# Performance work log

Measured on AMD Instinct MI355X. Metric: run time of the kernel, lower is better.

## Reference

```python
import jax, jax.numpy as jnp
import numpy as np
from jax.ops import segment_sum

N_NODES = 100000
N_EDGES = 3200000
NUM_FEATURES = 256


def setup_inputs() -> dict:
    key = jax.random.key(0)
    ks = jax.random.split(key, 12)
    def lin(k, fan_in, fan_out):
        bound = 1.0 / np.sqrt(fan_in)
        kw, kb = jax.random.split(k)
        W = jax.random.uniform(kw, (fan_in, fan_out), jnp.float32, -bound, bound)
        b = jax.random.uniform(kb, (fan_out,), jnp.float32, -bound, bound)
        return W, b
    x = jax.random.normal(ks[0], (N_NODES, NUM_FEATURES), jnp.float32)
    edge_index = jax.random.randint(ks[1], (2, N_EDGES), 0, N_NODES, jnp.int64 if jax.config.jax_enable_x64 else jnp.int32)
    W1, b1 = lin(ks[2], NUM_FEATURES, 64)
    W2, b2 = lin(ks[3], 64, 32)
    W3, b3 = lin(ks[4], 32, 16)
    Ws02, bs02 = lin(ks[5], NUM_FEATURES, 32)
    Ws03, bs03 = lin(ks[6], NUM_FEATURES, 16)
    Ws13, bs13 = lin(ks[7], 64, 16)
    Wout, bout = lin(ks[8], 16, 1)
    return dict(x=x, edge_index=edge_index, W1=W1, b1=b1, W2=W2, b2=b2,
                W3=W3, b3=b3, Ws02=Ws02, bs02=bs02, Ws03=Ws03, bs03=bs03,
                Ws13=Ws13, bs13=bs13, Wout=Wout, bout=bout)


def _deg_inv_sqrt(edge_index, n_nodes):
    # gcn_norm with self-loops: degree counted at target nodes, +1 for self-loop
    dst = edge_index[1]
    deg = segment_sum(jnp.ones(edge_index.shape[1], jnp.float32), dst, num_segments=n_nodes) + 1.0
    return jnp.where(deg > 0, jax.lax.rsqrt(deg), 0.0)


def _gcn_conv(x, W, b, edge_index, dinv):
    # PyG GCNConv: h = x W; out[i] = sum_{j->i} dinv[j]*dinv[i]*h[j] + dinv[i]^2*h[i] + b
    src, dst = edge_index[0], edge_index[1]
    h = x @ W                                   # [N, out]
    norm = (dinv[src] * dinv[dst])[:, None]     # [E, 1]
    agg = segment_sum(h[src] * norm, dst, num_segments=x.shape[0])
    agg = agg + (dinv * dinv)[:, None] * h      # self-loop term
    return agg + b


def reference(x, edge_index, W1, b1, W2, b2, W3, b3,
              Ws02, bs02, Ws03, bs03, Ws13, bs13, Wout, bout):
    # Dropout in eval mode (identity).
    dinv = _deg_inv_sqrt(edge_index, x.shape[0])
    x1 = jax.nn.relu(_gcn_conv(x, W1, b1, edge_index, dinv))
    x2 = jax.nn.relu(_gcn_conv(x1, W2, b2, edge_index, dinv) + x @ Ws02 + bs02)
    x3 = jax.nn.relu(_gcn_conv(x2, W3, b3, edge_index, dinv)
                     + x @ Ws03 + bs03 + x1 @ Ws13 + bs13)
    return jax.nn.sigmoid(x3 @ Wout + bout)
```

## Files before the change

kernel.cpp:

```cpp
#include <hip/hip_runtime.h>
#include <hip/hip_bf16.h>
#include <math.h>


#define NBUCK_MAX 512
#define P1_CHUNK 8192
#define EPT 32
#define BCAP 9216

typedef __attribute__((ext_vector_type(8))) short bfrag;
typedef __attribute__((ext_vector_type(4))) float f4_t;

__device__ inline float uaf(unsigned u) { return __uint_as_float(u); }
__device__ inline ushort f2bf(float f) {
    __hip_bfloat16 b = __float2bfloat16(f);
    return *reinterpret_cast<ushort*>(&b);
}


__global__ __launch_bounds__(256) void bucket_hist_kernel(
    const int* __restrict__ dst, int E, int* __restrict__ bucket_count, int nbuckets)
{
    __shared__ int lhist[NBUCK_MAX];
    for (int i = threadIdx.x; i < nbuckets; i += 256) lhist[i] = 0;
    __syncthreads();
    const int stride = gridDim.x * 256;
    for (int e = blockIdx.x * 256 + threadIdx.x; e < E; e += stride)
        atomicAdd(&lhist[dst[e] >> 8], 1);
    __syncthreads();
    for (int i = threadIdx.x; i < nbuckets; i += 256) {
        int c = lhist[i];
        if (c) atomicAdd(&bucket_count[i], c);
    }
}

__global__ __launch_bounds__(512) void bucket_scan_kernel(
    const int* __restrict__ bucket_count, int* __restrict__ bucket_base,
    int* __restrict__ bucket_cursor, int nbuckets)
{
    __shared__ int tmp[512];
    const int tid = threadIdx.x;
    int v = (tid < nbuckets) ? bucket_count[tid] : 0;
    tmp[tid] = v;
    __syncthreads();
    for (int off = 1; off < 512; off <<= 1) {
        int t = (tid >= off) ? tmp[tid - off] : 0;
        __syncthreads();
        tmp[tid] += t;
        __syncthreads();
    }
    if (tid < nbuckets) {
        int base = tmp[tid] - v;
        bucket_base[tid]   = base;
        bucket_cursor[tid] = base;
    }
}

__global__ __launch_bounds__(256) void partition_kernel(
    const int* __restrict__ src, const int* __restrict__ dst, int E,
    int* __restrict__ bucket_cursor, unsigned int* __restrict__ keys, int nbuckets)
{
    __shared__ int hist[NBUCK_MAX];
    __shared__ int lofs[NBUCK_MAX];
    __shared__ int gbase[NBUCK_MAX];
    __shared__ int lcur[NBUCK_MAX];
    __shared__ int ssum[256];
    __shared__ unsigned int stage[P1_CHUNK];
    __shared__ int gidx[P1_CHUNK];

    const int tid = threadIdx.x;
    const int e0  = blockIdx.x * P1_CHUNK;
    const int nE  = min(P1_CHUNK, E - e0);

    for (int i = tid; i < NBUCK_MAX; i += 256) { hist[i] = 0; lcur[i] = 0; }
    __syncthreads();

    int myb[EPT];
    unsigned int mypk[EPT];
#pragma unroll
    for (int j = 0; j < EPT; ++j) {
        const int e = e0 + tid + j * 256;
        if (e < E) {
            const int d = dst[e];
            myb[j]  = d >> 8;
            mypk[j] = ((unsigned int)(d & 255) << 17) | (unsigned int)src[e];
            atomicAdd(&hist[myb[j]], 1);
        } else myb[j] = -1;
    }
    __syncthreads();

    int a0 = (2 * tid     < nbuckets) ? hist[2 * tid]     : 0;
    int a1 = (2 * tid + 1 < nbuckets) ? hist[2 * tid + 1] : 0;
    ssum[tid] = a0 + a1;
    __syncthreads();
    for (int off = 1; off < 256; off <<= 1) {
        int t = (tid >= off) ? ssum[tid - off] : 0;
        __syncthreads();
        ssum[tid] += t;
        __syncthreads();
    }
    const int ex = ssum[tid] - (a0 + a1);
    if (2 * tid     < nbuckets) lofs[2 * tid]     = ex;
    if (2 * tid + 1 < nbuckets) lofs[2 * tid + 1] = ex + a0;
    __syncthreads();

    for (int i = tid; i < nbuckets; i += 256)
        gbase[i] = atomicAdd(&bucket_cursor[i], hist[i]);
    __syncthreads();

#pragma unroll
    for (int j = 0; j < EPT; ++j) {
        if (myb[j] >= 0) {
            const int b = myb[j];
            const int l = lofs[b] + atomicAdd(&lcur[b], 1);
            stage[l] = mypk[j];
            gidx[l]  = gbase[b] - lofs[b] + l;
        }
    }
    __syncthreads();

    for (int i = tid; i < nE; i += 256)
        keys[gidx[i]] = stage[i];
}

__global__ __launch_bounds__(256) void csr_build_kernel(
    const unsigned int* __restrict__ keys, const int* __restrict__ bucket_base,
    const int* __restrict__ bucket_count,
    int* __restrict__ row_off, float* __restrict__ dinv, int* __restrict__ col,
    int N, int E)
{
    __shared__ unsigned int inb[BCAP];
    __shared__ int outv[BCAP];
    __shared__ int hist[256];
    __shared__ int lofs[256];
    __shared__ int ssum[256];

    const int tid  = threadIdx.x;
    const int b    = blockIdx.x;
    const int base = bucket_base[b];
    const int cnt  = min(bucket_count[b], BCAP);
    const int n0   = b << 8;
    const int nn   = min(256, N - n0);

    for (int i = tid; i < cnt; i += 256) inb[i] = keys[base + i];
    hist[tid] = 0;
    __syncthreads();

    for (int i = tid; i < cnt; i += 256)
        atomicAdd(&hist[inb[i] >> 17], 1);
    __syncthreads();

    ssum[tid] = hist[tid];
    __syncthreads();
    for (int off = 1; off < 256; off <<= 1) {
        int t = (tid >= off) ? ssum[tid - off] : 0;
        __syncthreads();
        ssum[tid] += t;
        __syncthreads();
    }
    lofs[tid] = ssum[tid] - hist[tid];

    if (tid < nn) {
        row_off[n0 + tid] = base + lofs[tid];
        dinv[n0 + tid]    = rsqrtf((float)hist[tid] + 1.0f);
    }
    if (b == 0 && tid == 0) row_off[N] = E;
    __syncthreads();

    hist[tid] = 0;
    __syncthreads();

    for (int i = tid; i < cnt; i += 256) {
        const unsigned int k = inb[i];
        const int node = k >> 17;
        const int l = lofs[node] + atomicAdd(&hist[node], 1);
        outv[l] = (int)(k & 0x1FFFF);
    }
    __syncthreads();

    for (int i = tid; i < cnt; i += 256)
        col[base + i] = outv[i];
}


__global__ __launch_bounds__(256) void prep_weights_kernel(
    const float* __restrict__ W1, const float* __restrict__ Ws02,
    const float* __restrict__ Ws03, const float* __restrict__ W2,
    const float* __restrict__ Ws13, const float* __restrict__ W3,
    ushort* __restrict__ Wt0, ushort* __restrict__ Wt1, ushort* __restrict__ Wt2)
{
    int idx = blockIdx.x * 256 + threadIdx.x;
    if (idx < 32768) {
        int f = idx >> 8, k = idx & 255;
        float v = 0.f;
        if (f < 64)       v = W1[k * 64 + f];
        else if (f < 96)  v = Ws02[k * 32 + (f - 64)];
        else if (f < 112) v = Ws03[k * 16 + (f - 96)];
        Wt0[idx] = f2bf(v);
    } else if (idx < 32768 + 3072) {
        int t = idx - 32768;
        int f = t >> 6, k = t & 63;
        float v = (f < 32) ? W2[k * 32 + f] : Ws13[k * 16 + (f - 32)];
        Wt1[t] = f2bf(v);
    } else if (idx < 32768 + 3072 + 512) {
        int t = idx - 32768 - 3072;
        int f = t >> 5, k = t & 31;
        Wt2[t] = f2bf(W3[k * 16 + f]);
    }
}


__global__ __launch_bounds__(256, 4) void gemm_mfma0(
    const float* __restrict__ X, const ushort* __restrict__ Wt0,
    const float* __restrict__ bs02, const float* __restrict__ bs03,
    const float* __restrict__ dinv,
    __hip_bfloat16* __restrict__ g1, float* __restrict__ pre2,
    float* __restrict__ pre3, int N)
{
    constexpr int LDA = 40;
    __shared__ ushort As[2][128 * LDA];

    const int tid  = threadIdx.x;
    const int lane = tid & 63;
    const int wave = tid >> 6;
    const int n0   = blockIdx.x * 128;

    const int srow = tid >> 1;
    const int sq   = (tid & 1) * 4;
    const float* xrow = (n0 + srow < N) ? &X[(size_t)(n0 + srow) * 256] : nullptr;

    float4 pf[4];
#pragma unroll
    for (int j = 0; j < 4; ++j)
        pf[j] = xrow ? *reinterpret_cast<const float4*>(&xrow[(sq + j) * 4])
                     : make_float4(0.f, 0.f, 0.f, 0.f);

    f4_t acc[4][4];
#pragma unroll
    for (int a = 0; a < 4; ++a)
#pragma unroll
        for (int b = 0; b < 4; ++b) acc[a][b] = {0.f, 0.f, 0.f, 0.f};

    const int wm = wave & 1, wf = wave >> 1;
    const int mrow = (lane & 15);
    const int kq   = (lane >> 4) * 8;

    {
        ushort* dst = &As[0][srow * LDA + sq * 4];
#pragma unroll
        for (int j = 0; j < 4; ++j) {
            ushort4 cv;
            cv.x = f2bf(pf[j].x); cv.y = f2bf(pf[j].y);
            cv.z = f2bf(pf[j].z); cv.w = f2bf(pf[j].w);
            *reinterpret_cast<ushort4*>(&dst[j * 4]) = cv;
        }
    }
    __syncthreads();

    for (int panel = 0; panel < 8; ++panel) {
        const int kc = panel * 32;
        const int buf = panel & 1;

        if (panel < 7) {
#pragma unroll
            for (int j = 0; j < 4; ++j)
                pf[j] = xrow ? *reinterpret_cast<const float4*>(
                                   &xrow[(panel + 1) * 32 + (sq + j) * 4])
                             : make_float4(0.f, 0.f, 0.f, 0.f);
        }

        bfrag bfr[4];
#pragma unroll
        for (int ft = 0; ft < 4; ++ft) {
            const uint4 raw = *reinterpret_cast<const uint4*>(
                &Wt0[(size_t)(wf * 64 + ft * 16 + mrow) * 256 + kc + kq]);
            bfr[ft] = *reinterpret_cast<const bfrag*>(&raw);
        }
        bfrag af[4];
#pragma unroll
        for (int mt = 0; mt < 4; ++mt)
            af[mt] = *reinterpret_cast<const bfrag*>(
                &As[buf][(wm * 64 + mt * 16 + mrow) * LDA + kq]);
#pragma unroll
        for (int mt = 0; mt < 4; ++mt)
#pragma unroll
            for (int ft = 0; ft < 4; ++ft)
                acc[mt][ft] = __builtin_amdgcn_mfma_f32_16x16x32_bf16(
                    af[mt], bfr[ft], acc[mt][ft], 0, 0, 0);

        if (panel < 7) {
            ushort* dst = &As[1 - buf][srow * LDA + sq * 4];
#pragma unroll
            for (int j = 0; j < 4; ++j) {
                ushort4 cv;
                cv.x = f2bf(pf[j].x); cv.y = f2bf(pf[j].y);
                cv.z = f2bf(pf[j].z); cv.w = f2bf(pf[j].w);
                *reinterpret_cast<ushort4*>(&dst[j * 4]) = cv;
            }
            __syncthreads();
        }
    }

#pragma unroll
    for (int mt = 0; mt < 4; ++mt) {
#pragma unroll
        for (int ft = 0; ft < 4; ++ft) {
            const int fg = wf * 64 + ft * 16 + mrow;
#pragma unroll
            for (int r = 0; r < 4; ++r) {
                const int n = n0 + wm * 64 + mt * 16 + (lane >> 4) * 4 + r;
                if (n >= N) continue;
                const float a = acc[mt][ft][r];
                if (fg < 64) {
                    g1[(size_t)n * 64 + fg] = __float2bfloat16(dinv[n] * a);
                } else if (fg < 96) {
                    pre2[(size_t)n * 32 + (fg - 64)] = a + bs02[fg - 64];
                } else if (fg < 112) {
                    pre3[(size_t)n * 16 + (fg - 96)] = a + bs03[fg - 96];
                }
            }
        }
    }
}

__global__ __launch_bounds__(256) void gemm_mfma1(
    const ushort* __restrict__ X1, const ushort* __restrict__ Wt1,
    const float* __restrict__ bs13, const float* __restrict__ dinv,
    __hip_bfloat16* __restrict__ g2, float* __restrict__ pre3, int N)
{
    constexpr int LDA = 72;
    __shared__ ushort As[128 * LDA];

    const int tid  = threadIdx.x;
    const int lane = tid & 63;
    const int wave = tid >> 6;
    const int n0   = blockIdx.x * 128;

    for (int idx = tid; idx < 1024; idx += 256) {
        const int row = idx >> 3, c = idx & 7;
        const int n = n0 + row;
        uint4 v = make_uint4(0, 0, 0, 0);
        if (n < N) v = *reinterpret_cast<const uint4*>(&X1[(size_t)n * 64 + c * 8]);
        *reinterpret_cast<uint4*>(&As[row * LDA + c * 8]) = v;
    }
    __syncthreads();

    f4_t acc[2][3];
#pragma unroll
    for (int a = 0; a < 2; ++a)
#pragma unroll
        for (int b = 0; b < 3; ++b) acc[a][b] = {0.f, 0.f, 0.f, 0.f};

    const int m0 = wave * 32;
    const int mrow = lane & 15;
    const int kq   = (lane >> 4) * 8;
#pragma unroll
    for (int p = 0; p < 2; ++p) {
        bfrag af[2], bfr[3];
#pragma unroll
        for (int mt = 0; mt < 2; ++mt)
            af[mt] = *reinterpret_cast<const bfrag*>(
                &As[(m0 + mt * 16 + mrow) * LDA + p * 32 + kq]);
#pragma unroll
        for (int ft = 0; ft < 3; ++ft) {
            const uint4 raw = *reinterpret_cast<const uint4*>(
                &Wt1[(size_t)(ft * 16 + mrow) * 64 + p * 32 + kq]);
            bfr[ft] = *reinterpret_cast<const bfrag*>(&raw);
        }
#pragma unroll
        for (int mt = 0; mt < 2; ++mt)
#pragma unroll
            for (int ft = 0; ft < 3; ++ft)
                acc[mt][ft] = __builtin_amdgcn_mfma_f32_16x16x32_bf16(
                    af[mt], bfr[ft], acc[mt][ft], 0, 0, 0);
    }

#pragma unroll
    for (int mt = 0; mt < 2; ++mt) {
#pragma unroll
        for (int ft = 0; ft < 3; ++ft) {
            const int fg = ft * 16 + mrow;
#pragma unroll
            for (int r = 0; r < 4; ++r) {
                const int n = n0 + m0 + mt * 16 + (lane >> 4) * 4 + r;
                if (n >= N) continue;
                const float a = acc[mt][ft][r];
                if (fg < 32) {
                    g2[(size_t)n * 32 + fg] = __float2bfloat16(dinv[n] * a);
                } else {
                    pre3[(size_t)n * 16 + (fg - 32)] += a + bs13[fg - 32];
                }
            }
        }
    }
}

__global__ __launch_bounds__(256) void gemm_mfma2(
    const ushort* __restrict__ X2, const ushort* __restrict__ Wt2,
    const float* __restrict__ dinv, __hip_bfloat16* __restrict__ g3, int N)
{
    constexpr int LDA = 40;
    __shared__ ushort As[256 * LDA];

    const int tid  = threadIdx.x;
    const int lane = tid & 63;
    const int wave = tid >> 6;
    const int n0   = blockIdx.x * 256;

    for (int idx = tid; idx < 1024; idx += 256) {
        const int row = idx >> 2, c = idx & 3;
        const int n = n0 + row;
        uint4 v = make_uint4(0, 0, 0, 0);
        if (n < N) v = *reinterpret_cast<const uint4*>(&X2[(size_t)n * 32 + c * 8]);
        *reinterpret_cast<uint4*>(&As[row * LDA + c * 8]) = v;
    }
    __syncthreads();

    f4_t acc[4];
#pragma unroll
    for (int a = 0; a < 4; ++a) acc[a] = {0.f, 0.f, 0.f, 0.f};

    const int m0 = wave * 64;
    const int mrow = lane & 15;
    const int kq   = (lane >> 4) * 8;
    const uint4 raw = *reinterpret_cast<const uint4*>(&Wt2[(size_t)mrow * 32 + kq]);
    const bfrag bfr = *reinterpret_cast<const bfrag*>(&raw);
#pragma unroll
    for (int mt = 0; mt < 4; ++mt) {
        const bfrag af = *reinterpret_cast<const bfrag*>(
            &As[(m0 + mt * 16 + mrow) * LDA + kq]);
        acc[mt] = __builtin_amdgcn_mfma_f32_16x16x32_bf16(af, bfr, acc[mt], 0, 0, 0);
    }

#pragma unroll
    for (int mt = 0; mt < 4; ++mt) {
#pragma unroll
        for (int r = 0; r < 4; ++r) {
            const int n = n0 + m0 + mt * 16 + (lane >> 4) * 4 + r;
            if (n >= N) continue;
            g3[(size_t)n * 16 + mrow] = __float2bfloat16(dinv[n] * acc[mt][r]);
        }
    }
}


template<int F, int MODE>
__global__ __launch_bounds__(256) void agg_kernel(
    const ushort* __restrict__ g, const float* __restrict__ dinv,
    const int* __restrict__ row_off, const int* __restrict__ col,
    const float* __restrict__ bias, const float* __restrict__ pre,
    const float* __restrict__ Wout, const float* __restrict__ bout,
    void* __restrict__ out, int N)
{
    constexpr int FG  = F / 4;
    constexpr int EPW = 64 / FG;
    constexpr int U   = (F == 64) ? 4 : (F == 32 ? 2 : 1);

    const int lane = threadIdx.x & 63;
    const int wv   = threadIdx.x >> 6;
    const int i    = blockIdx.x * 4 + wv;
    if (i >= N) return;

    const int fg = lane % FG;
    const int eo = lane / FG;
    const int fb = fg * 4;

    float a0 = 0.f, a1 = 0.f, a2 = 0.f, a3 = 0.f;
    const int s = row_off[i], e = row_off[i + 1];
    int p = s + eo;
    for (; p + (U - 1) * EPW < e; p += U * EPW) {
        int js[U];
#pragma unroll
        for (int u = 0; u < U; ++u) js[u] = col[p + u * EPW];
        uint2 w[U];
#pragma unroll
        for (int u = 0; u < U; ++u)
            w[u] = *reinterpret_cast<const uint2*>(&g[(size_t)js[u] * F + fb]);
#pragma unroll
        for (int u = 0; u < U; ++u) {
            a0 += uaf(w[u].x << 16);
            a1 += uaf(w[u].x & 0xffff0000u);
            a2 += uaf(w[u].y << 16);
            a3 += uaf(w[u].y & 0xffff0000u);
        }
    }
    for (; p < e; p += EPW) {
        const uint2 w0 = *reinterpret_cast<const uint2*>(&g[(size_t)col[p] * F + fb]);
        a0 += uaf(w0.x << 16);
        a1 += uaf(w0.x & 0xffff0000u);
        a2 += uaf(w0.y << 16);
        a3 += uaf(w0.y & 0xffff0000u);
    }
#pragma unroll
    for (int off = FG; off < 64; off <<= 1) {
        a0 += __shfl_xor(a0, off);
        a1 += __shfl_xor(a1, off);
        a2 += __shfl_xor(a2, off);
        a3 += __shfl_xor(a3, off);
    }

    const uint2 ws = *reinterpret_cast<const uint2*>(&g[(size_t)i * F + fb]);
    const float di = dinv[i];
    float v0 = di * (a0 + uaf(ws.x << 16))        + bias[fb + 0];
    float v1 = di * (a1 + uaf(ws.x & 0xffff0000u)) + bias[fb + 1];
    float v2 = di * (a2 + uaf(ws.y << 16))        + bias[fb + 2];
    float v3 = di * (a3 + uaf(ws.y & 0xffff0000u)) + bias[fb + 3];
    if (MODE != 0) {
        const float4 pv = *reinterpret_cast<const float4*>(&pre[(size_t)i * F + fb]);
        v0 += pv.x; v1 += pv.y; v2 += pv.z; v3 += pv.w;
    }
    v0 = fmaxf(v0, 0.f); v1 = fmaxf(v1, 0.f);
    v2 = fmaxf(v2, 0.f); v3 = fmaxf(v3, 0.f);

    if (MODE != 2) {
        if (lane < FG) {
            uint2 o;
            o.x = (unsigned)f2bf(v0) | ((unsigned)f2bf(v1) << 16);
            o.y = (unsigned)f2bf(v2) | ((unsigned)f2bf(v3) << 16);
            *reinterpret_cast<uint2*>(&((ushort*)out)[(size_t)i * F + fb]) = o;
        }
    } else {
        float t = v0 * Wout[fb] + v1 * Wout[fb + 1] +
                  v2 * Wout[fb + 2] + v3 * Wout[fb + 3];
        t += __shfl_xor(t, 1);
        t += __shfl_xor(t, 2);
        if (lane == 0)
            ((float*)out)[i] = 1.0f / (1.0f + expf(-(t + bout[0])));
    }
}


extern "C" void kernel_launch(void* const* d_in, const int* in_sizes, int n_in,
                              void* d_out, int out_size, void* d_ws, size_t ws_size,
                              hipStream_t stream)
{
    const float* x    = (const float*)d_in[0];
    const int*   edge = (const int*)d_in[1];
    const float* W1   = (const float*)d_in[2];
    const float* b1   = (const float*)d_in[3];
    const float* W2   = (const float*)d_in[4];
    const float* b2   = (const float*)d_in[5];
    const float* W3   = (const float*)d_in[6];
    const float* b3   = (const float*)d_in[7];
    const float* Ws02 = (const float*)d_in[8];
    const float* bs02 = (const float*)d_in[9];
    const float* Ws03 = (const float*)d_in[10];
    const float* bs03 = (const float*)d_in[11];
    const float* Ws13 = (const float*)d_in[12];
    const float* bs13 = (const float*)d_in[13];
    const float* Wout = (const float*)d_in[14];
    const float* bout = (const float*)d_in[15];

    const int N = in_sizes[0] / 256;
    const int E = in_sizes[1] / 2;
    const int* srcv = edge;
    const int* dstv = edge + E;
    const int nbuckets = (N + 255) >> 8;

    char* ws = (char*)d_ws;
    size_t off = 0;
    auto alloc = [&](size_t bytes) -> void* {
        void* p = ws + off;
        off += (bytes + 255) & ~(size_t)255;
        return p;
    };
    unsigned int* keys = (unsigned int*)alloc((size_t)E * 4);
    int*   col      = (int*)  alloc((size_t)E * 4);
    int*   bcount   = (int*)  alloc((size_t)NBUCK_MAX * 4);
    int*   bbase    = (int*)  alloc((size_t)NBUCK_MAX * 4);
    int*   bcursor  = (int*)  alloc((size_t)NBUCK_MAX * 4);
    int*   row_off  = (int*)  alloc((size_t)(N + 1) * 4);
    float* dinv     = (float*)alloc((size_t)N * 4);
    ushort* Wt0     = (ushort*)alloc((size_t)128 * 256 * 2);
    ushort* Wt1     = (ushort*)alloc((size_t)48 * 64 * 2);
    ushort* Wt2     = (ushort*)alloc((size_t)16 * 32 * 2);
    ushort* g1      = (ushort*)alloc((size_t)N * 64 * 2);
    ushort* x1      = (ushort*)alloc((size_t)N * 64 * 2);
    ushort* g2      = (ushort*)alloc((size_t)N * 32 * 2);
    ushort* x2      = (ushort*)alloc((size_t)N * 32 * 2);
    ushort* g3      = (ushort*)alloc((size_t)N * 16 * 2);
    float* pre2     = (float*)alloc((size_t)N * 32 * 4);
    float* pre3     = (float*)alloc((size_t)N * 16 * 4);

    prep_weights_kernel<<<142, 256, 0, stream>>>(W1, Ws02, Ws03, W2, Ws13, W3,
                                                 Wt0, Wt1, Wt2);
    hipMemsetAsync(bcount, 0, (size_t)NBUCK_MAX * 4, stream);
    bucket_hist_kernel<<<1024, 256, 0, stream>>>(dstv, E, bcount, nbuckets);
    bucket_scan_kernel<<<1, 512, 0, stream>>>(bcount, bbase, bcursor, nbuckets);
    partition_kernel<<<(E + P1_CHUNK - 1) / P1_CHUNK, 256, 0, stream>>>(
        srcv, dstv, E, bcursor, keys, nbuckets);
    csr_build_kernel<<<nbuckets, 256, 0, stream>>>(
        keys, bbase, bcount, row_off, dinv, col, N, E);

    const int ab = (N + 3) / 4;

    gemm_mfma0<<<(N + 127) / 128, 256, 0, stream>>>(
        x, Wt0, bs02, bs03, dinv, (__hip_bfloat16*)g1, pre2, pre3, N);
    agg_kernel<64, 0><<<ab, 256, 0, stream>>>(g1, dinv, row_off, col,
                                              b1, nullptr, nullptr, nullptr, x1, N);
    gemm_mfma1<<<(N + 127) / 128, 256, 0, stream>>>(
        x1, Wt1, bs13, dinv, (__hip_bfloat16*)g2, pre3, N);
    agg_kernel<32, 1><<<ab, 256, 0, stream>>>(g2, dinv, row_off, col,
                                              b2, pre2, nullptr, nullptr, x2, N);
    gemm_mfma2<<<(N + 255) / 256, 256, 0, stream>>>(
        x2, Wt2, dinv, (__hip_bfloat16*)g3, N);
    agg_kernel<16, 2><<<ab, 256, 0, stream>>>(g3, dinv, row_off, col,
                                              b3, pre3, Wout, bout, d_out, N);
}
```

Baseline: 477.9 us.

## Load GEMM A-fragments directly from global memory, drop LDS staging, deepen aggregation unroll

The three MFMA GEMM kernels stop staging activations through shared memory and instead load each lane's A-fragment straight from global memory. The first GEMM converts fp32 to bf16 in registers and uses 64-row blocks, with each wave covering 32 output features across all rows. This removes the LDS writes, the barriers and the double buffering, and raises occupancy. In exchange each wave re-reads the same X rows, adding redundant global traffic that the L2 has to absorb. The neighbor-aggregation unroll factor is also doubled to keep more gather loads in flight.

Measured after the change: 486.3 us. Within noise of the previous version (+1.8%).

```diff
diff --git a/kernel.cpp b/kernel.cpp
--- a/kernel.cpp
+++ b/kernel.cpp
@@ -15,6 +15,16 @@
 __device__ inline ushort f2bf(float f) {
     __hip_bfloat16 b = __float2bfloat16(f);
     return *reinterpret_cast<ushort*>(&b);
+}
+__device__ inline bfrag cvt8(const float4 a, const float4 b) {
+    union { ushort u[8]; bfrag f; } r;
+    r.u[0] = f2bf(a.x); r.u[1] = f2bf(a.y); r.u[2] = f2bf(a.z); r.u[3] = f2bf(a.w);
+    r.u[4] = f2bf(b.x); r.u[5] = f2bf(b.y); r.u[6] = f2bf(b.z); r.u[7] = f2bf(b.w);
+    return r.f;
+}
+__device__ inline bfrag ld_bfrag(const ushort* p) {
+    const uint4 raw = *reinterpret_cast<const uint4*>(p);
+    return *reinterpret_cast<const bfrag*>(&raw);
 }
 
 
@@ -217,98 +227,60 @@
     __hip_bfloat16* __restrict__ g1, float* __restrict__ pre2,
     float* __restrict__ pre3, int N)
 {
-    constexpr int LDA = 40;
-    __shared__ ushort As[2][128 * LDA];
-
     const int tid  = threadIdx.x;
     const int lane = tid & 63;
-    const int wave = tid >> 6;
-    const int n0   = blockIdx.x * 128;
-
-    const int srow = tid >> 1;
-    const int sq   = (tid & 1) * 4;
-    const float* xrow = (n0 + srow < N) ? &X[(size_t)(n0 + srow) * 256] : nullptr;
-
-    float4 pf[4];
-#pragma unroll
-    for (int j = 0; j < 4; ++j)
-        pf[j] = xrow ? *reinterpret_cast<const float4*>(&xrow[(sq + j) * 4])
-                     : make_float4(0.f, 0.f, 0.f, 0.f);
-
-    f4_t acc[4][4];
+    const int wf   = tid >> 6;
+    const int n0   = blockIdx.x * 64;
+    const int mrow = lane & 15;
+    const int kq   = (lane >> 4) * 8;
+
+    f4_t acc[4][2];
 #pragma unroll
     for (int a = 0; a < 4; ++a)
 #pragma unroll
-        for (int b = 0; b < 4; ++b) acc[a][b] = {0.f, 0.f, 0.f, 0.f};
-
-    const int wm = wave & 1, wf = wave >> 1;
-    const int mrow = (lane & 15);
-    const int kq   = (lane >> 4) * 8;
-
-    {
-        ushort* dst = &As[0][srow * LDA + sq * 4];
-#pragma unroll
-        for (int j = 0; j < 4; ++j) {
-            ushort4 cv;
-            cv.x = f2bf(pf[j].x); cv.y = f2bf(pf[j].y);
-            cv.z = f2bf(pf[j].z); cv.w = f2bf(pf[j].w);
-            *reinterpret_cast<ushort4*>(&dst[j * 4]) = cv;
-        }
-    }
-    __syncthreads();
-
-    for (int panel = 0; panel < 8; ++panel) {
-        const int kc = panel * 32;
-        const int buf = panel & 1;
-
-        if (panel < 7) {
-#pragma unroll
-            for (int j = 0; j < 4; ++j)
-                pf[j] = xrow ? *reinterpret_cast<const float4*>(
-                                   &xrow[(panel + 1) * 32 + (sq + j) * 4])
-                             : make_float4(0.f, 0.f, 0.f, 0.f);
-        }
-
-        bfrag bfr[4];
-#pragma unroll
-        for (int ft = 0; ft < 4; ++ft) {
-            const uint4 raw = *reinterpret_cast<const uint4*>(
-                &Wt0[(size_t)(wf * 64 + ft * 16 + mrow) * 256 + kc + kq]);
-            bfr[ft] = *reinterpret_cast<const bfrag*>(&raw);
-        }
+        for (int b = 0; b < 2; ++b) acc[a][b] = {0.f, 0.f, 0.f, 0.f};
+
+    const float* xrow[4];
+#pragma unroll
+    for (int mt = 0; mt < 4; ++mt) {
+        int r = n0 + mt * 16 + mrow;
+        r = (r < N) ? r : (N - 1);
+        xrow[mt] = &X[(size_t)r * 256 + kq];
+    }
+    const ushort* wrow[2];
+#pragma unroll
+    for (int ft = 0; ft < 2; ++ft)
+        wrow[ft] = &Wt0[(size_t)(wf * 32 + ft * 16 + mrow) * 256 + kq];
+
+#pragma unroll
+    for (int p = 0; p < 8; ++p) {
+        bfrag bf[2];
+#pragma unroll
+        for (int ft = 0; ft < 2; ++ft)
+            bf[ft] = ld_bfrag(&wrow[ft][p * 32]);
         bfrag af[4];
 #pragma unroll
+        for (int mt = 0; mt < 4; ++mt) {
+            const float4 u0 = *reinterpret_cast<const float4*>(&xrow[mt][p * 32]);
+            const float4 u1 = *reinterpret_cast<const float4*>(&xrow[mt][p * 32 + 4]);
+            af[mt] = cvt8(u0, u1);
+        }
+#pragma unroll
         for (int mt = 0; mt < 4; ++mt)
-            af[mt] = *reinterpret_cast<const bfrag*>(
-                &As[buf][(wm * 64 + mt * 16 + mrow) * LDA + kq]);
-#pragma unroll
-        for (int mt = 0; mt < 4; ++mt)
-#pragma unroll
-            for (int ft = 0; ft < 4; ++ft)
+#pragma unroll
+            for (int ft = 0; ft < 2; ++ft)
                 acc[mt][ft] = __builtin_amdgcn_mfma_f32_16x16x32_bf16(
-                    af[mt], bfr[ft], acc[mt][ft], 0, 0, 0);
-
-        if (panel < 7) {
-            ushort* dst = &As[1 - buf][srow * LDA + sq * 4];
-#pragma unroll
-            for (int j = 0; j < 4; ++j) {
-                ushort4 cv;
-                cv.x = f2bf(pf[j].x); cv.y = f2bf(pf[j].y);
-                cv.z = f2bf(pf[j].z); cv.w = f2bf(pf[j].w);
-                *reinterpret_cast<ushort4*>(&dst[j * 4]) = cv;
-            }
-            __syncthreads();
-        }
+                    af[mt], bf[ft], acc[mt][ft], 0, 0, 0);
     }
 
 #pragma unroll
     for (int mt = 0; mt < 4; ++mt) {
 #pragma unroll
-        for (int ft = 0; ft < 4; ++ft) {
-            const int fg = wf * 64 + ft * 16 + mrow;
+        for (int ft = 0; ft < 2; ++ft) {
+            const int fg = wf * 32 + ft * 16 + mrow;
 #pragma unroll
             for (int r = 0; r < 4; ++r) {
-                const int n = n0 + wm * 64 + mt * 16 + (lane >> 4) * 4 + r;
+                const int n = n0 + mt * 16 + (lane >> 4) * 4 + r;
                 if (n >= N) continue;
                 const float a = acc[mt][ft][r];
                 if (fg < 64) {
@@ -328,51 +300,44 @@
     const float* __restrict__ bs13, const float* __restrict__ dinv,
     __hip_bfloat16* __restrict__ g2, float* __restrict__ pre3, int N)
 {
-    constexpr int LDA = 72;
-    __shared__ ushort As[128 * LDA];
-
     const int tid  = threadIdx.x;
     const int lane = tid & 63;
     const int wave = tid >> 6;
-    const int n0   = blockIdx.x * 128;
-
-    for (int idx = tid; idx < 1024; idx += 256) {
-        const int row = idx >> 3, c = idx & 7;
-        const int n = n0 + row;
-        uint4 v = make_uint4(0, 0, 0, 0);
-        if (n < N) v = *reinterpret_cast<const uint4*>(&X1[(size_t)n * 64 + c * 8]);
-        *reinterpret_cast<uint4*>(&As[row * LDA + c * 8]) = v;
-    }
-    __syncthreads();
-
-    f4_t acc[2][3];
-#pragma unroll
-    for (int a = 0; a < 2; ++a)
-#pragma unroll
-        for (int b = 0; b < 3; ++b) acc[a][b] = {0.f, 0.f, 0.f, 0.f};
-
-    const int m0 = wave * 32;
+    const int n0   = blockIdx.x * 128 + wave * 32;
     const int mrow = lane & 15;
     const int kq   = (lane >> 4) * 8;
+
+    f4_t acc[2][3];
+#pragma unroll
+    for (int a = 0; a < 2; ++a)
+#pragma unroll
+        for (int b = 0; b < 3; ++b) acc[a][b] = {0.f, 0.f, 0.f, 0.f};
+
+    const ushort* xrow[2];
+#pragma unroll
+    for (int mt = 0; mt < 2; ++mt) {
+        int r = n0 + mt * 16 + mrow;
+        r = (r < N) ? r : (N - 1);
+        xrow[mt] = &X1[(size_t)r * 64 + kq];
+    }
+    const ushort* wrow[3];
+#pragma unroll
+    for (int ft = 0; ft < 3; ++ft)
+        wrow[ft] = &Wt1[(size_t)(ft * 16 + mrow) * 64 + kq];
+
 #pragma unroll
     for (int p = 0; p < 2; ++p) {
-        bfrag af[2], bfr[3];
-#pragma unroll
-        for (int mt = 0; mt < 2; ++mt)
-            af[mt] = *reinterpret_cast<const bfrag*>(
-                &As[(m0 + mt * 16 + mrow) * LDA + p * 32 + kq]);
-#pragma unroll
-        for (int ft = 0; ft < 3; ++ft) {
-            const uint4 raw = *reinterpret_cast<const uint4*>(
-                &Wt1[(size_t)(ft * 16 + mrow) * 64 + p * 32 + kq]);
-            bfr[ft] = *reinterpret_cast<const bfrag*>(&raw);
-        }
+        bfrag af[2], bf[3];
+#pragma unroll
+        for (int mt = 0; mt < 2; ++mt) af[mt] = ld_bfrag(&xrow[mt][p * 32]);
+#pragma unroll
+        for (int ft = 0; ft < 3; ++ft) bf[ft] = ld_bfrag(&wrow[ft][p * 32]);
 #pragma unroll
         for (int mt = 0; mt < 2; ++mt)
 #pragma unroll
             for (int ft = 0; ft < 3; ++ft)
                 acc[mt][ft] = __builtin_amdgcn_mfma_f32_16x16x32_bf16(
-                    af[mt], bfr[ft], acc[mt][ft], 0, 0, 0);
+                    af[mt], bf[ft], acc[mt][ft], 0, 0, 0);
     }
 
 #pragma unroll
@@ -382,7 +347,7 @@
             const int fg = ft * 16 + mrow;
 #pragma unroll
             for (int r = 0; r < 4; ++r) {
-                const int n = n0 + m0 + mt * 16 + (lane >> 4) * 4 + r;
+                const int n = n0 + mt * 16 + (lane >> 4) * 4 + r;
                 if (n >= N) continue;
                 const float a = acc[mt][ft][r];
                 if (fg < 32) {
@@ -399,44 +364,31 @@
     const ushort* __restrict__ X2, const ushort* __restrict__ Wt2,
     const float* __restrict__ dinv, __hip_bfloat16* __restrict__ g3, int N)
 {
-    constexpr int LDA = 40;
-    __shared__ ushort As[256 * LDA];
-
     const int tid  = threadIdx.x;
     const int lane = tid & 63;
     const int wave = tid >> 6;
-    const int n0   = blockIdx.x * 256;
-
-    for (int idx = tid; idx < 1024; idx += 256) {
-        const int row = idx >> 2, c = idx & 3;
-        const int n = n0 + row;
-        uint4 v = make_uint4(0, 0, 0, 0);
-        if (n < N) v = *reinterpret_cast<const uint4*>(&X2[(size_t)n * 32 + c * 8]);
-        *reinterpret_cast<uint4*>(&As[row * LDA + c * 8]) = v;
-    }
-    __syncthreads();
-
-    f4_t acc[4];
-#pragma unroll
-    for (int a = 0; a < 4; ++a) acc[a] = {0.f, 0.f, 0.f, 0.f};
-
-    const int m0 = wave * 64;
+    const int n0   = blockIdx.x * 128 + wave * 32;
     const int mrow = lane & 15;
     const int kq   = (lane >> 4) * 8;
-    const uint4 raw = *reinterpret_cast<const uint4*>(&Wt2[(size_t)mrow * 32 + kq]);
-    const bfrag bfr = *reinterpret_cast<const bfrag*>(&raw);
-#pragma unroll
-    for (int mt = 0; mt < 4; ++mt) {
-        const bfrag af = *reinterpret_cast<const bfrag*>(
-            &As[(m0 + mt * 16 + mrow) * LDA + kq]);
-        acc[mt] = __builtin_amdgcn_mfma_f32_16x16x32_bf16(af, bfr, acc[mt], 0, 0, 0);
-    }
-
-#pragma unroll
-    for (int mt = 0; mt < 4; ++mt) {
+
+    f4_t acc[2];
+#pragma unroll
+    for (int a = 0; a < 2; ++a) acc[a] = {0.f, 0.f, 0.f, 0.f};
+
+    const bfrag bf = ld_bfrag(&Wt2[(size_t)mrow * 32 + kq]);
+#pragma unroll
+    for (int mt = 0; mt < 2; ++mt) {
+        int r = n0 + mt * 16 + mrow;
+        r = (r < N) ? r : (N - 1);
+        const bfrag af = ld_bfrag(&X2[(size_t)r * 32 + kq]);
+        acc[mt] = __builtin_amdgcn_mfma_f32_16x16x32_bf16(af, bf, acc[mt], 0, 0, 0);
+    }
+
+#pragma unroll
+    for (int mt = 0; mt < 2; ++mt) {
 #pragma unroll
         for (int r = 0; r < 4; ++r) {
-            const int n = n0 + m0 + mt * 16 + (lane >> 4) * 4 + r;
+            const int n = n0 + mt * 16 + (lane >> 4) * 4 + r;
             if (n >= N) continue;
             g3[(size_t)n * 16 + mrow] = __float2bfloat16(dinv[n] * acc[mt][r]);
         }
@@ -454,7 +406,7 @@
 {
     constexpr int FG  = F / 4;
     constexpr int EPW = 64 / FG;
-    constexpr int U   = (F == 64) ? 4 : (F == 32 ? 2 : 1);
+    constexpr int U   = (F == 64) ? 8 : (F == 32 ? 4 : 2);
 
     const int lane = threadIdx.x & 63;
     const int wv   = threadIdx.x >> 6;
@@ -501,9 +453,9 @@
 
     const uint2 ws = *reinterpret_cast<const uint2*>(&g[(size_t)i * F + fb]);
     const float di = dinv[i];
-    float v0 = di * (a0 + uaf(ws.x << 16))        + bias[fb + 0];
+    float v0 = di * (a0 + uaf(ws.x << 16))         + bias[fb + 0];
     float v1 = di * (a1 + uaf(ws.x & 0xffff0000u)) + bias[fb + 1];
-    float v2 = di * (a2 + uaf(ws.y << 16))        + bias[fb + 2];
+    float v2 = di * (a2 + uaf(ws.y << 16))         + bias[fb + 2];
     float v3 = di * (a3 + uaf(ws.y & 0xffff0000u)) + bias[fb + 3];
     if (MODE != 0) {
         const float4 pv = *reinterpret_cast<const float4*>(&pre[(size_t)i * F + fb]);
@@ -594,7 +546,7 @@
 
     const int ab = (N + 3) / 4;
 
-    gemm_mfma0<<<(N + 127) / 128, 256, 0, stream>>>(
+    gemm_mfma0<<<(N + 63) / 64, 256, 0, stream>>>(
         x, Wt0, bs02, bs03, dinv, (__hip_bfloat16*)g1, pre2, pre3, N);
     agg_kernel<64, 0><<<ab, 256, 0, stream>>>(g1, dinv, row_off, col,
                                               b1, nullptr, nullptr, nullptr, x1, N);
@@ -602,7 +554,7 @@
         x1, Wt1, bs13, dinv, (__hip_bfloat16*)g2, pre3, N);
     agg_kernel<32, 1><<<ab, 256, 0, stream>>>(g2, dinv, row_off, col,
                                               b2, pre2, nullptr, nullptr, x2, N);
-    gemm_mfma2<<<(N + 255) / 256, 256, 0, stream>>>(
+    gemm_mfma2<<<(N + 127) / 128, 256, 0, stream>>>(
         x2, Wt2, dinv, (__hip_bfloat16*)g3, N);
     agg_kernel<16, 2><<<ab, 256, 0, stream>>>(g3, dinv, row_off, col,
                                               b3, pre3, Wout, bout, d_out, N);
```
